# Kernel tuning notes

Measured on AMD Instinct MI355X. Metric: run time of the kernel, lower is better.

The kernel has to match this reference:

```python
import jax, jax.numpy as jnp
import numpy as np

HIDDEN = 512
HEADS = 8
HEAD_DIM = HIDDEN // HEADS


def setup_inputs() -> dict:
    key = jax.random.key(0)
    ks = jax.random.split(key, 13)
    B, S, H = 4, 2048, HIDDEN
    s = 1.0 / np.sqrt(H).astype(np.float32)
    inp = {
        "values": jax.random.normal(ks[0], (B, S, H), jnp.float32),
        "keys": jax.random.normal(ks[1], (B, S, H), jnp.float32),
        "query": jax.random.normal(ks[2], (B, S, H), jnp.float32),
        "mask": jax.random.randint(ks[3], (B, S), 0, 2, jnp.int32),
        "Wq": jax.random.normal(ks[4], (H, H), jnp.float32) * s,
        "bq": jnp.zeros((H,), jnp.float32),
        "Wk": jax.random.normal(ks[5], (H, H), jnp.float32) * s,
        "bk": jnp.zeros((H,), jnp.float32),
        "Wv": jax.random.normal(ks[6], (H, H), jnp.float32) * s,
        "bv": jnp.zeros((H,), jnp.float32),
        "Wo": jax.random.normal(ks[7], (H, H), jnp.float32) * s,
        "bo": jnp.zeros((H,), jnp.float32),
    }
    return inp


def reference(values, keys, query, mask, Wq, bq, Wk, bk, Wv, bv, Wo, bo):
    B, Sq, H = query.shape
    Sk = keys.shape[1]
    # projections (x @ W + b)
    Q = query @ Wq + bq
    K = keys @ Wk + bk
    V = values @ Wv + bv
    # [B, S, H] -> [B, heads, S, head_dim]
    def split(x, S):
        return x.reshape(B, S, HEADS, HEAD_DIM).transpose(0, 2, 1, 3)
    Qh, Kh, Vh = split(Q, Sq), split(K, Sk), split(V, Sk)
    scale = 1.0 / np.sqrt(HEAD_DIM).astype(np.float32)
    scores = jnp.einsum('bhqd,bhkd->bhqk', Qh, Kh) * scale  # [B,H,Sq,Sk]
    m = mask[:, None, None, :]  # [B,1,1,Sk]
    scores = jnp.where(m == 0, jnp.float32(-1e9), scores)
    attn = jax.nn.softmax(scores, axis=-1)
    ctx = jnp.einsum('bhqk,bhkd->bhqd', attn, Vh)
    ctx = ctx.transpose(0, 2, 1, 3).reshape(B, Sq, H)
    return ctx @ Wo + bo
```

## Files before the change

kernel.cpp:

```cpp
#include <hip/hip_runtime.h>

#define HID 512
#define NH 8
#define HD 64
#define BATCH 4
#define SEQ 2048
#define MTOT (BATCH * SEQ)

typedef unsigned short ushort_t;
typedef __bf16 bf16x8 __attribute__((ext_vector_type(8)));
typedef unsigned short ushort8v __attribute__((ext_vector_type(8)));
typedef unsigned short ushort4v __attribute__((ext_vector_type(4)));
typedef float floatx4 __attribute__((ext_vector_type(4)));
typedef int intx4 __attribute__((ext_vector_type(4)));

static __device__ __forceinline__ unsigned short f2bf(float f) {
  union { float f; unsigned int u; } c; c.f = f;
  unsigned int u = c.u;
  u += 0x7fff + ((u >> 16) & 1);
  return (unsigned short)(u >> 16);
}
static __device__ __forceinline__ float bf2f(unsigned short s) {
  union { unsigned int u; float f; } c; c.u = ((unsigned int)s) << 16;
  return c.f;
}
static __device__ __forceinline__ bf16x8 asbf(ushort8v v) {
  return __builtin_bit_cast(bf16x8, v);
}

__global__ void detect_dtype(const unsigned int* __restrict__ q, int* __restrict__ flag) {
  if (threadIdx.x == 0 && blockIdx.x == 0) {
    int hits = 0;
    for (int i = 0; i < 256; ++i) {
      unsigned e = (q[i] >> 7) & 0xff;
      hits += (e >= 110 && e <= 136) ? 1 : 0;
    }
    flag[0] = (hits >= 128) ? 1 : 0;
  }
}

__global__ __launch_bounds__(256) void prep_w(
    const void* __restrict__ W0, const void* __restrict__ W1,
    const void* __restrict__ W2, const void* __restrict__ W3,
    ushort_t* __restrict__ T0, ushort_t* __restrict__ T1,
    ushort_t* __restrict__ T2, ushort_t* __restrict__ T3,
    const int* __restrict__ flag) {
  const int isbf = flag[0];
  const void* W; ushort_t* T;
  switch (blockIdx.y) {
    case 0: W = W0; T = T0; break;
    case 1: W = W1; T = T1; break;
    case 2: W = W2; T = T2; break;
    default: W = W3; T = T3; break;
  }
  int idx = blockIdx.x * 256 + threadIdx.x;
  int k = idx >> 9, n = idx & 511;
  ushort_t v = isbf ? ((const ushort_t*)W)[k * HID + n]
                    : f2bf(((const float*)W)[k * HID + n]);
  T[n * HID + k] = v;
}

__global__ __launch_bounds__(256) void prep_b(
    const void* __restrict__ B0, const void* __restrict__ B1,
    const void* __restrict__ B2, const void* __restrict__ B3,
    float* __restrict__ biasF, const int* __restrict__ flag) {
  const int isbf = flag[0];
  int i = blockIdx.x * 256 + threadIdx.x;
  int t = i >> 9, j = i & 511;
  const void* B = (t == 0) ? B0 : (t == 1) ? B1 : (t == 2) ? B2 : B3;
  biasF[i] = isbf ? bf2f(((const ushort_t*)B)[j]) : ((const float*)B)[j];
}

__global__ __launch_bounds__(256) void gemm_qkv(
    const void* __restrict__ X0, const void* __restrict__ X1, const void* __restrict__ X2,
    const ushort_t* __restrict__ WtBase, const float* __restrict__ biasBase,
    ushort_t* __restrict__ YBase, const int* __restrict__ flag) {
  const int isbf = flag[0];
  const int z = blockIdx.z;
  const void* X = (z == 0) ? X0 : (z == 1) ? X1 : X2;
  const ushort_t* Wt = WtBase + (size_t)z * HID * HID;
  const float* biasF = biasBase + (size_t)z * HID;
  ushort_t* Y = YBase + (size_t)z * MTOT * HID;

  const int tid = threadIdx.x;
  const int wid = tid >> 6, lane = tid & 63;
  const int id = lane & 15, quad = lane >> 4;
  const int wm = wid >> 1, wn = wid & 1;
  const int m0 = blockIdx.x * 64, n0 = blockIdx.y * 128;

  __shared__ ushort_t At[64 * 72];
  __shared__ ushort_t Bt[128 * 72];

  const int srow = tid >> 3;
  const int scol = (tid & 7) * 8;

  floatx4 acc[2][4];
#pragma unroll
  for (int i = 0; i < 2; ++i)
#pragma unroll
    for (int j = 0; j < 4; ++j) acc[i][j] = (floatx4){0.f, 0.f, 0.f, 0.f};

  for (int k0 = 0; k0 < HID; k0 += 64) {
    ushort8v aR[2], bR[4];
    if (isbf) {
      const ushort_t* ap = (const ushort_t*)X + (long)(m0 + srow) * HID + k0 + scol;
#pragma unroll
      for (int p = 0; p < 2; ++p) aR[p] = *(const ushort8v*)(ap + (long)p * 32 * HID);
    } else {
      const float* apf = (const float*)X + (long)(m0 + srow) * HID + k0 + scol;
#pragma unroll
      for (int p = 0; p < 2; ++p) {
        floatx4 f0 = *(const floatx4*)(apf + (long)p * 32 * HID);
        floatx4 f1 = *(const floatx4*)(apf + (long)p * 32 * HID + 4);
#pragma unroll
        for (int i = 0; i < 4; ++i) { aR[p][i] = f2bf(f0[i]); aR[p][4 + i] = f2bf(f1[i]); }
      }
    }
    {
      const ushort_t* bp = Wt + (long)(n0 + srow) * HID + k0 + scol;
#pragma unroll
      for (int p = 0; p < 4; ++p) bR[p] = *(const ushort8v*)(bp + (long)p * 32 * HID);
    }
    __syncthreads();
#pragma unroll
    for (int p = 0; p < 2; ++p) *(ushort8v*)(&At[(srow + 32 * p) * 72 + scol]) = aR[p];
#pragma unroll
    for (int p = 0; p < 4; ++p) *(ushort8v*)(&Bt[(srow + 32 * p) * 72 + scol]) = bR[p];
    __syncthreads();
#pragma unroll
    for (int kk = 0; kk < 64; kk += 32) {
      ushort8v af[2], bf4[4];
#pragma unroll
      for (int ms = 0; ms < 2; ++ms) af[ms] = *(const ushort8v*)(&At[(wm * 32 + ms * 16 + id) * 72 + kk + quad * 8]);
#pragma unroll
      for (int ns = 0; ns < 4; ++ns) bf4[ns] = *(const ushort8v*)(&Bt[(wn * 64 + ns * 16 + id) * 72 + kk + quad * 8]);
#pragma unroll
      for (int ms = 0; ms < 2; ++ms)
#pragma unroll
        for (int ns = 0; ns < 4; ++ns)
          acc[ms][ns] = __builtin_amdgcn_mfma_f32_16x16x32_bf16(asbf(af[ms]), asbf(bf4[ns]), acc[ms][ns], 0, 0, 0);
    }
  }
#pragma unroll
  for (int ns = 0; ns < 4; ++ns) {
    float bv = biasF[n0 + wn * 64 + ns * 16 + id];
    int col = n0 + wn * 64 + ns * 16 + id;
#pragma unroll
    for (int ms = 0; ms < 2; ++ms) {
      int row0 = m0 + wm * 32 + ms * 16 + quad * 4;
#pragma unroll
      for (int r = 0; r < 4; ++r)
        Y[(long)(row0 + r) * HID + col] = f2bf(acc[ms][ns][r] + bv);
    }
  }
}

__global__ __launch_bounds__(256) void gemm_lds_out(
    const ushort_t* __restrict__ X, const ushort_t* __restrict__ Wt,
    const float* __restrict__ biasF, void* __restrict__ out,
    const int* __restrict__ flag) {
  const int isbf = flag[0];
  const int tid = threadIdx.x;
  const int wid = tid >> 6, lane = tid & 63;
  const int id = lane & 15, quad = lane >> 4;
  const int wm = wid >> 1, wn = wid & 1;
  const int m0 = blockIdx.x * 64, n0 = blockIdx.y * 128;

  __shared__ ushort_t At[64 * 72];
  __shared__ ushort_t Bt[128 * 72];

  const int srow = tid >> 3;
  const int scol = (tid & 7) * 8;

  floatx4 acc[2][4];
#pragma unroll
  for (int i = 0; i < 2; ++i)
#pragma unroll
    for (int j = 0; j < 4; ++j) acc[i][j] = (floatx4){0.f, 0.f, 0.f, 0.f};

  for (int k0 = 0; k0 < HID; k0 += 64) {
    ushort8v aR[2], bR[4];
    {
      const ushort_t* ap = X + (long)(m0 + srow) * HID + k0 + scol;
#pragma unroll
      for (int p = 0; p < 2; ++p) aR[p] = *(const ushort8v*)(ap + (long)p * 32 * HID);
      const ushort_t* bp = Wt + (long)(n0 + srow) * HID + k0 + scol;
#pragma unroll
      for (int p = 0; p < 4; ++p) bR[p] = *(const ushort8v*)(bp + (long)p * 32 * HID);
    }
    __syncthreads();
#pragma unroll
    for (int p = 0; p < 2; ++p) *(ushort8v*)(&At[(srow + 32 * p) * 72 + scol]) = aR[p];
#pragma unroll
    for (int p = 0; p < 4; ++p) *(ushort8v*)(&Bt[(srow + 32 * p) * 72 + scol]) = bR[p];
    __syncthreads();
#pragma unroll
    for (int kk = 0; kk < 64; kk += 32) {
      ushort8v af[2], bf4[4];
#pragma unroll
      for (int ms = 0; ms < 2; ++ms) af[ms] = *(const ushort8v*)(&At[(wm * 32 + ms * 16 + id) * 72 + kk + quad * 8]);
#pragma unroll
      for (int ns = 0; ns < 4; ++ns) bf4[ns] = *(const ushort8v*)(&Bt[(wn * 64 + ns * 16 + id) * 72 + kk + quad * 8]);
#pragma unroll
      for (int ms = 0; ms < 2; ++ms)
#pragma unroll
        for (int ns = 0; ns < 4; ++ns)
          acc[ms][ns] = __builtin_amdgcn_mfma_f32_16x16x32_bf16(asbf(af[ms]), asbf(bf4[ns]), acc[ms][ns], 0, 0, 0);
    }
  }
#pragma unroll
  for (int ns = 0; ns < 4; ++ns) {
    float bv = biasF[n0 + wn * 64 + ns * 16 + id];
    int col = n0 + wn * 64 + ns * 16 + id;
#pragma unroll
    for (int ms = 0; ms < 2; ++ms) {
      int row0 = m0 + wm * 32 + ms * 16 + quad * 4;
      if (isbf) {
        ushort_t* o = (ushort_t*)out;
#pragma unroll
        for (int r = 0; r < 4; ++r) o[(long)(row0 + r) * HID + col] = f2bf(acc[ms][ns][r] + bv);
      } else {
        float* o = (float*)out;
#pragma unroll
        for (int r = 0; r < 4; ++r) o[(long)(row0 + r) * HID + col] = acc[ms][ns][r] + bv;
      }
    }
  }
}

__global__ __launch_bounds__(256) void flash_attn(
    const ushort_t* __restrict__ Q, const ushort_t* __restrict__ K,
    const ushort_t* __restrict__ V, const int* __restrict__ mask,
    ushort_t* __restrict__ ctx) {
  const int qblk = blockIdx.x, h = blockIdx.y, b = blockIdx.z;
  const int tid = threadIdx.x;
  const int wid = tid >> 6, lane = tid & 63;
  const int id = lane & 15, quad = lane >> 4;

  __shared__ ushort_t Kt[64 * 72];
  __shared__ ushort_t Vt[64 * 72];
  __shared__ ushort_t Pl[4][32 * 72];

  const ushort_t* Qb = Q + (long)(b * SEQ + qblk * 128 + wid * 32) * HID + h * HD;
  const ushort_t* Kb = K + (long)(b * SEQ) * HID + h * HD;
  const ushort_t* Vb = V + (long)(b * SEQ) * HID + h * HD;
  const int* mrow = mask + b * SEQ;

  ushort8v qf[2][2];
#pragma unroll
  for (int qs = 0; qs < 2; ++qs)
#pragma unroll
    for (int kh = 0; kh < 2; ++kh)
      qf[qs][kh] = *(const ushort8v*)(Qb + (qs * 16 + id) * HID + kh * 32 + quad * 8);

  floatx4 o[4][2];
  float m_i[2] = {-1e30f, -1e30f}, l_i[2] = {0.f, 0.f};
#pragma unroll
  for (int dg = 0; dg < 4; ++dg) { o[dg][0] = (floatx4){0,0,0,0}; o[dg][1] = (floatx4){0,0,0,0}; }

  const int skey = tid >> 2;
  const int sdc  = (tid & 3) * 16;
  const int vkp  = (tid & 31) * 2;
  const int vdc  = (tid >> 5) * 8;

  for (int kb = 0; kb < SEQ / 64; ++kb) {
    {
      const ushort_t* kpp = Kb + (long)(kb * 64 + skey) * HID + sdc;
      ushort8v k0v = *(const ushort8v*)(kpp);
      ushort8v k1v = *(const ushort8v*)(kpp + 8);
      *(ushort8v*)(&Kt[skey * 72 + sdc])     = k0v;
      *(ushort8v*)(&Kt[skey * 72 + sdc + 8]) = k1v;
      const ushort_t* vp0 = Vb + (long)(kb * 64 + vkp) * HID + vdc;
      ushort8v v0v = *(const ushort8v*)(vp0);
      ushort8v v1v = *(const ushort8v*)(vp0 + HID);
#pragma unroll
      for (int i = 0; i < 8; ++i) {
        unsigned int dw = (unsigned int)v0v[i] | ((unsigned int)v1v[i] << 16);
        *(unsigned int*)(&Vt[(vdc + i) * 72 + vkp]) = dw;
      }
    }
    __syncthreads();

    floatx4 st[2][4];
#pragma unroll
    for (int ks = 0; ks < 4; ++ks) {
      ushort8v kf0 = *(const ushort8v*)(&Kt[(ks * 16 + id) * 72 + quad * 8]);
      ushort8v kf1 = *(const ushort8v*)(&Kt[(ks * 16 + id) * 72 + 32 + quad * 8]);
#pragma unroll
      for (int qs = 0; qs < 2; ++qs) {
        floatx4 a = (floatx4){0,0,0,0};
        a = __builtin_amdgcn_mfma_f32_16x16x32_bf16(asbf(kf0), asbf(qf[qs][0]), a, 0, 0, 0);
        a = __builtin_amdgcn_mfma_f32_16x16x32_bf16(asbf(kf1), asbf(qf[qs][1]), a, 0, 0, 0);
        st[qs][ks] = a;
      }
    }
#pragma unroll
    for (int ks = 0; ks < 4; ++ks) {
      intx4 mv = *(const intx4*)(mrow + kb * 64 + ks * 16 + quad * 4);
#pragma unroll
      for (int r = 0; r < 4; ++r) {
        float s0 = st[0][ks][r] * 0.125f, s1 = st[1][ks][r] * 0.125f;
        st[0][ks][r] = mv[r] ? s0 : -1e9f;
        st[1][ks][r] = mv[r] ? s1 : -1e9f;
      }
    }
#pragma unroll
    for (int qs = 0; qs < 2; ++qs) {
      float mx = st[qs][0][0];
#pragma unroll
      for (int ks = 0; ks < 4; ++ks)
#pragma unroll
        for (int r = 0; r < 4; ++r) mx = fmaxf(mx, st[qs][ks][r]);
      mx = fmaxf(mx, __shfl_xor(mx, 16));
      mx = fmaxf(mx, __shfl_xor(mx, 32));
      float mnew = fmaxf(m_i[qs], mx);
      float alpha = __expf(m_i[qs] - mnew);
      float rs = 0.f;
#pragma unroll
      for (int ks = 0; ks < 4; ++ks) {
        ushort4v pk;
#pragma unroll
        for (int r = 0; r < 4; ++r) {
          float p = __expf(st[qs][ks][r] - mnew);
          rs += p;
          pk[r] = f2bf(p);
        }
        *(ushort4v*)(&Pl[wid][(qs * 16 + id) * 72 + ks * 16 + quad * 4]) = pk;
      }
      rs += __shfl_xor(rs, 16);
      rs += __shfl_xor(rs, 32);
      l_i[qs] = l_i[qs] * alpha + rs;
      m_i[qs] = mnew;
#pragma unroll
      for (int dg = 0; dg < 4; ++dg) o[dg][qs] *= alpha;
    }
    __syncthreads();

#pragma unroll
    for (int kc = 0; kc < 2; ++kc) {
      ushort8v pf0 = *(const ushort8v*)(&Pl[wid][(0 * 16 + id) * 72 + kc * 32 + quad * 8]);
      ushort8v pf1 = *(const ushort8v*)(&Pl[wid][(1 * 16 + id) * 72 + kc * 32 + quad * 8]);
#pragma unroll
      for (int dg = 0; dg < 4; ++dg) {
        ushort8v vf = *(const ushort8v*)(&Vt[(dg * 16 + id) * 72 + kc * 32 + quad * 8]);
        o[dg][0] = __builtin_amdgcn_mfma_f32_16x16x32_bf16(asbf(vf), asbf(pf0), o[dg][0], 0, 0, 0);
        o[dg][1] = __builtin_amdgcn_mfma_f32_16x16x32_bf16(asbf(vf), asbf(pf1), o[dg][1], 0, 0, 0);
      }
    }
    __syncthreads();
  }

#pragma unroll
  for (int qs = 0; qs < 2; ++qs) {
    float inv = 1.0f / l_i[qs];
    long qrow = (long)(b * SEQ + qblk * 128 + wid * 32 + qs * 16 + id);
#pragma unroll
    for (int dg = 0; dg < 4; ++dg) {
      ushort4v pk;
#pragma unroll
      for (int r = 0; r < 4; ++r) pk[r] = f2bf(o[dg][qs][r] * inv);
      *(ushort4v*)(&ctx[qrow * HID + h * HD + dg * 16 + quad * 4]) = pk;
    }
  }
}

extern "C" void kernel_launch(void* const* d_in, const int* in_sizes, int n_in,
                              void* d_out, int out_size, void* d_ws, size_t ws_size,
                              hipStream_t stream) {
  const void* values = d_in[0];
  const void* keys   = d_in[1];
  const void* query  = d_in[2];
  const int*  mask   = (const int*)d_in[3];
  const void* Wq = d_in[4];  const void* bq = d_in[5];
  const void* Wk = d_in[6];  const void* bk = d_in[7];
  const void* Wv = d_in[8];  const void* bv = d_in[9];
  const void* Wo = d_in[10]; const void* bo = d_in[11];

  ushort_t* ws = (ushort_t*)d_ws;
  const size_t NEL = (size_t)MTOT * HID;
  ushort_t* Qp  = ws;
  ushort_t* Kp  = ws + NEL;
  ushort_t* Vp  = ws + 2 * NEL;
  ushort_t* Cp  = ws + 3 * NEL;
  ushort_t* WqT = ws + 4 * NEL;
  ushort_t* WkT = WqT + (size_t)HID * HID;
  ushort_t* WvT = WkT + (size_t)HID * HID;
  ushort_t* WoT = WvT + (size_t)HID * HID;
  float* biasF  = (float*)(WoT + (size_t)HID * HID);
  int* flag     = (int*)(biasF + 4 * HID);

  detect_dtype<<<1, 64, 0, stream>>>((const unsigned int*)query, flag);
  prep_w<<<dim3(1024, 4), 256, 0, stream>>>(Wq, Wk, Wv, Wo, WqT, WkT, WvT, WoT, flag);
  prep_b<<<8, 256, 0, stream>>>(bq, bk, bv, bo, biasF, flag);

  gemm_qkv<<<dim3(MTOT / 64, HID / 128, 3), 256, 0, stream>>>(
      query, keys, values, WqT, biasF, Qp, flag);

  flash_attn<<<dim3(SEQ / 128, NH, BATCH), 256, 0, stream>>>(Qp, Kp, Vp, mask, Cp);

  gemm_lds_out<<<dim3(MTOT / 64, HID / 128), 256, 0, stream>>>(
      Cp, WoT, biasF + 3 * HID, d_out, flag);
}
```

Baseline: 251.5 us.

## Prefetch K/V tiles, use exp2 with mask bias, lazy softmax rescale in attention

```diff
diff --git a/kernel.cpp b/kernel.cpp
--- a/kernel.cpp
+++ b/kernel.cpp
@@ -12,13 +12,10 @@
 typedef unsigned short ushort8v __attribute__((ext_vector_type(8)));
 typedef unsigned short ushort4v __attribute__((ext_vector_type(4)));
 typedef float floatx4 __attribute__((ext_vector_type(4)));
-typedef int intx4 __attribute__((ext_vector_type(4)));
 
 static __device__ __forceinline__ unsigned short f2bf(float f) {
-  union { float f; unsigned int u; } c; c.f = f;
-  unsigned int u = c.u;
-  u += 0x7fff + ((u >> 16) & 1);
-  return (unsigned short)(u >> 16);
+  __bf16 b = (__bf16)f;
+  return __builtin_bit_cast(unsigned short, b);
 }
 static __device__ __forceinline__ float bf2f(unsigned short s) {
   union { unsigned int u; float f; } c; c.u = ((unsigned int)s) << 16;
@@ -27,6 +24,11 @@
 static __device__ __forceinline__ bf16x8 asbf(ushort8v v) {
   return __builtin_bit_cast(bf16x8, v);
 }
+static __device__ __forceinline__ float max3f(float a, float b, float c) {
+  return fmaxf(fmaxf(a, b), c);
+}
+
+#define SC_LOG2E 0.18033688011112042f
 
 __global__ void detect_dtype(const unsigned int* __restrict__ q, int* __restrict__ flag) {
   if (threadIdx.x == 0 && blockIdx.x == 0) {
@@ -71,6 +73,12 @@
   biasF[i] = isbf ? bf2f(((const ushort_t*)B)[j]) : ((const float*)B)[j];
 }
 
+__global__ __launch_bounds__(256) void prep_mask(
+    const int* __restrict__ mask, float* __restrict__ mb) {
+  int i = blockIdx.x * 256 + threadIdx.x;
+  mb[i] = mask[i] ? 0.f : -1e9f;
+}
+
 __global__ __launch_bounds__(256) void gemm_qkv(
     const void* __restrict__ X0, const void* __restrict__ X1, const void* __restrict__ X2,
     const ushort_t* __restrict__ WtBase, const float* __restrict__ biasBase,
@@ -230,7 +238,7 @@
 
 __global__ __launch_bounds__(256) void flash_attn(
     const ushort_t* __restrict__ Q, const ushort_t* __restrict__ K,
-    const ushort_t* __restrict__ V, const int* __restrict__ mask,
+    const ushort_t* __restrict__ V, const float* __restrict__ mb,
     ushort_t* __restrict__ ctx) {
   const int qblk = blockIdx.x, h = blockIdx.y, b = blockIdx.z;
   const int tid = threadIdx.x;
@@ -244,7 +252,7 @@
   const ushort_t* Qb = Q + (long)(b * SEQ + qblk * 128 + wid * 32) * HID + h * HD;
   const ushort_t* Kb = K + (long)(b * SEQ) * HID + h * HD;
   const ushort_t* Vb = V + (long)(b * SEQ) * HID + h * HD;
-  const int* mrow = mask + b * SEQ;
+  const float* mrow = mb + b * SEQ;
 
   ushort8v qf[2][2];
 #pragma unroll
@@ -263,23 +271,34 @@
   const int vkp  = (tid & 31) * 2;
   const int vdc  = (tid >> 5) * 8;
 
+  ushort8v k0v, k1v, v0v, v1v;
+  {
+    const ushort_t* kpp = Kb + (long)skey * HID + sdc;
+    k0v = *(const ushort8v*)(kpp);
+    k1v = *(const ushort8v*)(kpp + 8);
+    const ushort_t* vp0 = Vb + (long)vkp * HID + vdc;
+    v0v = *(const ushort8v*)(vp0);
+    v1v = *(const ushort8v*)(vp0 + HID);
+  }
+
   for (int kb = 0; kb < SEQ / 64; ++kb) {
-    {
-      const ushort_t* kpp = Kb + (long)(kb * 64 + skey) * HID + sdc;
-      ushort8v k0v = *(const ushort8v*)(kpp);
-      ushort8v k1v = *(const ushort8v*)(kpp + 8);
-      *(ushort8v*)(&Kt[skey * 72 + sdc])     = k0v;
-      *(ushort8v*)(&Kt[skey * 72 + sdc + 8]) = k1v;
-      const ushort_t* vp0 = Vb + (long)(kb * 64 + vkp) * HID + vdc;
-      ushort8v v0v = *(const ushort8v*)(vp0);
-      ushort8v v1v = *(const ushort8v*)(vp0 + HID);
-#pragma unroll
-      for (int i = 0; i < 8; ++i) {
-        unsigned int dw = (unsigned int)v0v[i] | ((unsigned int)v1v[i] << 16);
-        *(unsigned int*)(&Vt[(vdc + i) * 72 + vkp]) = dw;
-      }
-    }
-    __syncthreads();
+    *(ushort8v*)(&Kt[skey * 72 + sdc])     = k0v;
+    *(ushort8v*)(&Kt[skey * 72 + sdc + 8]) = k1v;
+#pragma unroll
+    for (int i = 0; i < 8; ++i) {
+      unsigned int dw = (unsigned int)v0v[i] | ((unsigned int)v1v[i] << 16);
+      *(unsigned int*)(&Vt[(vdc + i) * 72 + vkp]) = dw;
+    }
+    __syncthreads();
+
+    if (kb + 1 < SEQ / 64) {
+      const ushort_t* kpp = Kb + (long)((kb + 1) * 64 + skey) * HID + sdc;
+      k0v = *(const ushort8v*)(kpp);
+      k1v = *(const ushort8v*)(kpp + 8);
+      const ushort_t* vp0 = Vb + (long)((kb + 1) * 64 + vkp) * HID + vdc;
+      v0v = *(const ushort8v*)(vp0);
+      v1v = *(const ushort8v*)(vp0 + HID);
+    }
 
     floatx4 st[2][4];
 #pragma unroll
@@ -296,32 +315,41 @@
     }
 #pragma unroll
     for (int ks = 0; ks < 4; ++ks) {
-      intx4 mv = *(const intx4*)(mrow + kb * 64 + ks * 16 + quad * 4);
+      floatx4 mbv = *(const floatx4*)(mrow + kb * 64 + ks * 16 + quad * 4);
 #pragma unroll
       for (int r = 0; r < 4; ++r) {
-        float s0 = st[0][ks][r] * 0.125f, s1 = st[1][ks][r] * 0.125f;
-        st[0][ks][r] = mv[r] ? s0 : -1e9f;
-        st[1][ks][r] = mv[r] ? s1 : -1e9f;
+        st[0][ks][r] = fmaf(st[0][ks][r], SC_LOG2E, mbv[r]);
+        st[1][ks][r] = fmaf(st[1][ks][r], SC_LOG2E, mbv[r]);
       }
     }
 #pragma unroll
     for (int qs = 0; qs < 2; ++qs) {
-      float mx = st[qs][0][0];
-#pragma unroll
-      for (int ks = 0; ks < 4; ++ks)
-#pragma unroll
-        for (int r = 0; r < 4; ++r) mx = fmaxf(mx, st[qs][ks][r]);
+      float a0 = max3f(st[qs][0][0], st[qs][0][1], st[qs][0][2]);
+      float a1 = max3f(st[qs][0][3], st[qs][1][0], st[qs][1][1]);
+      float a2 = max3f(st[qs][1][2], st[qs][1][3], st[qs][2][0]);
+      float a3 = max3f(st[qs][2][1], st[qs][2][2], st[qs][2][3]);
+      float a4 = max3f(st[qs][3][0], st[qs][3][1], st[qs][3][2]);
+      float mx = max3f(a0, a1, st[qs][3][3]);
+      float mz = max3f(a2, a3, a4);
+      mx = fmaxf(mx, mz);
       mx = fmaxf(mx, __shfl_xor(mx, 16));
       mx = fmaxf(mx, __shfl_xor(mx, 32));
-      float mnew = fmaxf(m_i[qs], mx);
-      float alpha = __expf(m_i[qs] - mnew);
+      if (!__all(mx - m_i[qs] <= 8.f)) {
+        float mnew = fmaxf(m_i[qs], mx);
+        float alpha = exp2f(m_i[qs] - mnew);
+        m_i[qs] = mnew;
+        l_i[qs] *= alpha;
+#pragma unroll
+        for (int dg = 0; dg < 4; ++dg) o[dg][qs] *= alpha;
+      }
+      float mcur = m_i[qs];
       float rs = 0.f;
 #pragma unroll
       for (int ks = 0; ks < 4; ++ks) {
         ushort4v pk;
 #pragma unroll
         for (int r = 0; r < 4; ++r) {
-          float p = __expf(st[qs][ks][r] - mnew);
+          float p = exp2f(st[qs][ks][r] - mcur);
           rs += p;
           pk[r] = f2bf(p);
         }
@@ -329,12 +357,8 @@
       }
       rs += __shfl_xor(rs, 16);
       rs += __shfl_xor(rs, 32);
-      l_i[qs] = l_i[qs] * alpha + rs;
-      m_i[qs] = mnew;
-#pragma unroll
-      for (int dg = 0; dg < 4; ++dg) o[dg][qs] *= alpha;
-    }
-    __syncthreads();
+      l_i[qs] += rs;
+    }
 
 #pragma unroll
     for (int kc = 0; kc < 2; ++kc) {
@@ -387,16 +411,18 @@
   ushort_t* WvT = WkT + (size_t)HID * HID;
   ushort_t* WoT = WvT + (size_t)HID * HID;
   float* biasF  = (float*)(WoT + (size_t)HID * HID);
-  int* flag     = (int*)(biasF + 4 * HID);
+  float* mbias  = biasF + 4 * HID;
+  int* flag     = (int*)(mbias + (size_t)BATCH * SEQ);
 
   detect_dtype<<<1, 64, 0, stream>>>((const unsigned int*)query, flag);
   prep_w<<<dim3(1024, 4), 256, 0, stream>>>(Wq, Wk, Wv, Wo, WqT, WkT, WvT, WoT, flag);
   prep_b<<<8, 256, 0, stream>>>(bq, bk, bv, bo, biasF, flag);
+  prep_mask<<<MTOT / 256, 256, 0, stream>>>(mask, mbias);
 
   gemm_qkv<<<dim3(MTOT / 64, HID / 128, 3), 256, 0, stream>>>(
       query, keys, values, WqT, biasF, Qp, flag);
 
-  flash_attn<<<dim3(SEQ / 128, NH, BATCH), 256, 0, stream>>>(Qp, Kp, Vp, mask, Cp);
+  flash_attn<<<dim3(SEQ / 128, NH, BATCH), 256, 0, stream>>>(Qp, Kp, Vp, mbias, Cp);
 
   gemm_lds_out<<<dim3(MTOT / 64, HID / 128), 256, 0, stream>>>(
       Cp, WoT, biasF + 3 * HID, d_out, flag);
```

New measurement: 240.5 us. 1.05x faster.
